# Optimization experiments

Measured on AMD Instinct MI355X. Metric: run time of the kernel, lower is better.

The kernel has to match this reference:

```python
import jax, jax.numpy as jnp
import numpy as np

ENC_H = 128
DEC_H = 256
DEC_STEPS = 10


def _gru_cell(x, h, Wih, Whh, bih, bhh):
    # PyTorch GRU cell, gate order (r, z, n)
    gi = x @ Wih.T + bih          # (B, 3H)
    gh = h @ Whh.T + bhh          # (B, 3H)
    H = h.shape[-1]
    ir, iz, inn = gi[:, :H], gi[:, H:2 * H], gi[:, 2 * H:]
    hr, hz, hn = gh[:, :H], gh[:, H:2 * H], gh[:, 2 * H:]
    r = jax.nn.sigmoid(ir + hr)
    z = jax.nn.sigmoid(iz + hz)
    n = jnp.tanh(inn + r * hn)
    return (1.0 - z) * n + z * h


def setup_inputs() -> dict:
    key = jax.random.key(0)
    ks = jax.random.split(key, 12)
    B, S = 4096, 128
    s = 0.1
    return {
        "x": jax.random.normal(ks[0], (B, S, 5), jnp.float32),
        "y": jax.random.normal(ks[1], (B, S, 1), jnp.float32),
        "enc_Wih": jax.random.normal(ks[2], (3 * ENC_H, 5), jnp.float32) * s,
        "enc_Whh": jax.random.normal(ks[3], (3 * ENC_H, ENC_H), jnp.float32) * s,
        "enc_bih": jax.random.normal(ks[4], (3 * ENC_H,), jnp.float32) * s,
        "enc_bhh": jax.random.normal(ks[5], (3 * ENC_H,), jnp.float32) * s,
        "dec_Wih": jax.random.normal(ks[6], (3 * DEC_H, ENC_H + 1), jnp.float32) * s,
        "dec_Whh": jax.random.normal(ks[7], (3 * DEC_H, DEC_H), jnp.float32) * s,
        "dec_bih": jax.random.normal(ks[8], (3 * DEC_H,), jnp.float32) * s,
        "dec_bhh": jax.random.normal(ks[9], (3 * DEC_H,), jnp.float32) * s,
        "lin_W": jax.random.normal(ks[10], (4, DEC_H), jnp.float32) * s,
        "lin_b": jax.random.normal(ks[11], (4,), jnp.float32) * s,
    }


def reference(x, y, enc_Wih, enc_Whh, enc_bih, enc_bhh,
              dec_Wih, dec_Whh, dec_bih, dec_bhh, lin_W, lin_b):
    B, S, _ = x.shape
    xs = jnp.transpose(x, (1, 0, 2))   # (S, B, 5)
    ys = jnp.transpose(y, (1, 0, 2))   # (S, B, 1)

    # Encoder: only the final hidden state (contex) is consumed downstream.
    h0 = jnp.zeros((B, ENC_H), x.dtype)

    def enc_step(h, xt):
        return _gru_cell(xt, h, enc_Wih, enc_Whh, enc_bih, enc_bhh), None

    contex, _ = jax.lax.scan(enc_step, h0, xs)   # (B, 128)

    # Decoder: initial hidden is ones (torch.ones_like(shape)), 10 steps.
    hdec0 = jnp.ones((B, DEC_H), x.dtype)

    def dec_step(h, yt):
        xt = jnp.concatenate([contex, yt], axis=-1)   # (B, 129)
        h2 = _gru_cell(xt, h, dec_Wih, dec_Whh, dec_bih, dec_bhh)
        out = h2 @ lin_W.T + lin_b                    # (B, 4)
        return h2, out

    _, outs = jax.lax.scan(dec_step, hdec0, ys[:DEC_STEPS])  # (10, B, 4)

    # res starts as ones; only first 10 rows written.
    res = jnp.ones((S, B, 4), x.dtype).at[:DEC_STEPS].set(outs)
    return jnp.transpose(res, (1, 0, 2))   # (B, S, 4)
```

## Files before the change

kernel.cpp:

```cpp
#include <hip/hip_runtime.h>

#define B_SZ 4096
#define S_SZ 128
#define XD 5
#define EH 128
#define DH 256
#define DSTEPS 10

typedef short v8s __attribute__((ext_vector_type(8)));
typedef float v4f __attribute__((ext_vector_type(4)));

__device__ __forceinline__ float bf2f(unsigned short u) {
    union { unsigned int i; float f; } v; v.i = ((unsigned int)u) << 16; return v.f;
}
__device__ __forceinline__ unsigned short f2bf(float f) {
    union { float f; unsigned int i; } v; v.f = f;
    unsigned int x = v.i;
    return (unsigned short)((x + 0x7FFFu + ((x >> 16) & 1u)) >> 16);
}
__device__ __forceinline__ float fexp2(float x) { return __builtin_amdgcn_exp2f(x); }
__device__ __forceinline__ float frcp(float x) { return __builtin_amdgcn_rcpf(x); }
__device__ __forceinline__ unsigned int cvt2bf(float lo, float hi) {
    unsigned int r;
    asm("v_cvt_pk_bf16_f32 %0, %1, %2" : "=v"(r) : "v"(lo), "v"(hi));
    return r;
}

#define SC_S (-1.44269504088896f)
#define SC_T ( 2.88539008177793f)

__global__ __launch_bounds__(256) void prep_kernel(
    const float* __restrict__ dWih,
    const float* __restrict__ dWhh,
    unsigned short* __restrict__ wihp,
    unsigned short* __restrict__ dWhh_bf)
{
    const int gsz = gridDim.x * 256;
    for (int i = blockIdx.x * 256 + threadIdx.x; i < 768 * 256; i += gsz) {
        const float sc = ((i >> 8) < 512) ? SC_S : SC_T;
        dWhh_bf[i] = f2bf(sc * dWhh[i]);
    }
    for (int i = blockIdx.x * 256 + threadIdx.x; i < 768 * 136; i += gsz) {
        int col = i / 136, k = i - col * 136;
        const float sc = (col < 512) ? SC_S : SC_T;
        wihp[i] = (k < 129) ? f2bf(sc * dWih[col * 129 + k]) : (unsigned short)0;
    }
}

__global__ __launch_bounds__(512, 2)
void fused_kernel(
    const float* __restrict__ x,
    const float* __restrict__ Wih32,
    const float* __restrict__ Whh32,
    const float* __restrict__ bih,
    const float* __restrict__ bhh,
    const float* __restrict__ dbih,
    const float* __restrict__ dbhh,
    const float* __restrict__ y,
    const unsigned short* __restrict__ wihp,
    const unsigned short* __restrict__ dWhh_bf,
    const float* __restrict__ linW,
    const float* __restrict__ linb,
    float* __restrict__ out)
{
    __shared__ __align__(16) char uni[118784];
    __shared__ unsigned short hb[2][16][136];
    __shared__ __align__(16) unsigned short zpad[8];
    __shared__ unsigned short hshf[32 * 16 * 8];
    __shared__ unsigned short lwf[32 * 16 * 8];
    __shared__ float ysh[16][DSTEPS];

    const int tid = threadIdx.x;
    const int bid = blockIdx.x;
    const int wv = tid >> 6;
    const int lane = tid & 63;
    const int n = lane & 15;
    const int kg = lane >> 4;
    const int r0 = bid * 16;

    {
        auto xs = (unsigned short (*)[16][8])uni;

        for (int i = tid; i < 2 * 16 * 136; i += 512) ((unsigned short*)hb)[i] = 0;
        if (tid < 8) zpad[tid] = 0;
        for (int i = tid; i < 16 * S_SZ * 8; i += 512) {
            int m = i >> 10;
            int rem = i & 1023;
            int t = rem >> 3;
            int j = rem & 7;
            unsigned short v = 0;
            if (j < XD) v = f2bf(x[(size_t)(r0 + m) * (S_SZ * XD) + t * XD + j]);
            else if (j == XD) v = 0x3F80;
            xs[t][m][j] = v;
        }

        const int colw = wv * 16 + n;
        v8s fw[3][4];
        v8s fx[3];
        #pragma unroll
        for (int g = 0; g < 3; ++g) {
            const float sc = (g < 2) ? SC_S : SC_T;
            const int gcol = g * EH + colw;
            #pragma unroll
            for (int kt = 0; kt < 4; ++kt) {
                const float* p = &Whh32[(size_t)gcol * EH + kt * 32 + kg * 8];
                float4 lo = *(const float4*)p;
                float4 hi = *(const float4*)(p + 4);
                v8s f;
                f[0] = (short)f2bf(sc * lo.x); f[1] = (short)f2bf(sc * lo.y);
                f[2] = (short)f2bf(sc * lo.z); f[3] = (short)f2bf(sc * lo.w);
                f[4] = (short)f2bf(sc * hi.x); f[5] = (short)f2bf(sc * hi.y);
                f[6] = (short)f2bf(sc * hi.z); f[7] = (short)f2bf(sc * hi.w);
                fw[g][kt] = f;
            }
            v8s t = {0, 0, 0, 0, 0, 0, 0, 0};
            if (kg == 0) {
                const float* p = &Wih32[gcol * XD];
                #pragma unroll
                for (int j = 0; j < XD; ++j) t[j] = (short)f2bf(sc * p[j]);
                float b = (g < 2) ? (sc * (bih[gcol] + bhh[gcol]))
                                  : (sc * bih[gcol]);
                t[XD] = (short)f2bf(b);
            }
            fx[g] = t;
        }
        const float bhn = SC_T * bhh[2 * EH + colw];

        const v4f vzero = {0.f, 0.f, 0.f, 0.f};
        float hst[4] = {0.f, 0.f, 0.f, 0.f};
        __syncthreads();

        #pragma unroll 2
        for (int t = 0; t < S_SZ; ++t) {
            const int p = t & 1;
            v8s a[4];
            #pragma unroll
            for (int kt = 0; kt < 4; ++kt)
                a[kt] = *(const v8s*)&hb[p][n][kt * 32 + kg * 8];
            const unsigned short* xsrc = (kg == 0) ? &xs[t][n][0] : &zpad[0];
            v8s ax = *(const v8s*)xsrc;

            v4f accr  = __builtin_amdgcn_mfma_f32_16x16x32_bf16(a[0], fw[0][0], vzero, 0, 0, 0);
            v4f accz  = __builtin_amdgcn_mfma_f32_16x16x32_bf16(a[0], fw[1][0], vzero, 0, 0, 0);
            v4f acchn = __builtin_amdgcn_mfma_f32_16x16x32_bf16(a[0], fw[2][0], vzero, 0, 0, 0);
            #pragma unroll
            for (int kt = 1; kt < 4; ++kt) {
                accr  = __builtin_amdgcn_mfma_f32_16x16x32_bf16(a[kt], fw[0][kt], accr, 0, 0, 0);
                accz  = __builtin_amdgcn_mfma_f32_16x16x32_bf16(a[kt], fw[1][kt], accz, 0, 0, 0);
                acchn = __builtin_amdgcn_mfma_f32_16x16x32_bf16(a[kt], fw[2][kt], acchn, 0, 0, 0);
            }
            accr = __builtin_amdgcn_mfma_f32_16x16x32_bf16(ax, fx[0], accr, 0, 0, 0);
            accz = __builtin_amdgcn_mfma_f32_16x16x32_bf16(ax, fx[1], accz, 0, 0, 0);
            v4f accin = __builtin_amdgcn_mfma_f32_16x16x32_bf16(ax, fx[2], vzero, 0, 0, 0);

            float hnew[4];
            #pragma unroll
            for (int e = 0; e < 4; ++e) {
                float r  = frcp(1.f + fexp2(accr[e]));
                float z  = frcp(1.f + fexp2(accz[e]));
                float nn = 1.f - 2.f * frcp(fexp2(accin[e] + r * (acchn[e] + bhn)) + 1.f);
                float h  = nn + z * (hst[e] - nn);
                hst[e] = h;
                hnew[e] = h;
            }
            const unsigned int pk01 = cvt2bf(hnew[0], hnew[1]);
            const unsigned int pk23 = cvt2bf(hnew[2], hnew[3]);
            hb[1 - p][kg * 4 + 0][colw] = (unsigned short)(pk01 & 0xFFFFu);
            hb[1 - p][kg * 4 + 1][colw] = (unsigned short)(pk01 >> 16);
            hb[1 - p][kg * 4 + 2][colw] = (unsigned short)(pk23 & 0xFFFFu);
            hb[1 - p][kg * 4 + 3][colw] = (unsigned short)(pk23 >> 16);
            __syncthreads();
        }
    }

    {
        const int w = wv;
        const int cbase = w * 32;
        const int rb = r0;
        float* gish = (float*)uni;
        float* wysh = (float*)(uni + 59392);

        {
            int col = tid >> 5, kgrp = tid & 31;
            unsigned short v8[8];
            #pragma unroll
            for (int j = 0; j < 8; ++j)
                v8[j] = (col < 4) ? f2bf(linW[col * 256 + kgrp * 8 + j]) : (unsigned short)0;
            *(uint4*)&lwf[(kgrp * 16 + col) * 8] = *(uint4*)v8;
        }
        if (tid < 16 * DSTEPS) {
            int row = tid / DSTEPS, tt = tid - row * DSTEPS;
            ysh[row][tt] = y[(size_t)(rb + row) * S_SZ + tt];
        }
        for (int i = tid; i < 32 * 16 * 8; i += 512) hshf[i] = 0x3F80;

        v8s fB[3][2][8];
        #pragma unroll
        for (int g = 0; g < 3; ++g)
            #pragma unroll
            for (int cg = 0; cg < 2; ++cg)
                #pragma unroll
                for (int kt = 0; kt < 8; ++kt)
                    fB[g][cg][kt] = *(const v8s*)
                        &dWhh_bf[(size_t)(g * DH + cbase + cg * 16 + n) * DH + kt * 32 + kg * 8];

        const v4f vzero = {0.f, 0.f, 0.f, 0.f};
        v4f gi[3][2];
        #pragma unroll
        for (int g = 0; g < 3; ++g)
            #pragma unroll
            for (int cg = 0; cg < 2; ++cg) gi[g][cg] = vzero;

        #pragma unroll
        for (int kt = 0; kt < 4; ++kt) {
            v8s actex = *(const v8s*)&hb[0][n][kt * 32 + kg * 8];
            #pragma unroll
            for (int g = 0; g < 3; ++g)
                #pragma unroll
                for (int cg = 0; cg < 2; ++cg) {
                    v8s bw = *(const v8s*)
                        &wihp[(size_t)(g * DH + cbase + cg * 16 + n) * 136 + kt * 32 + kg * 8];
                    gi[g][cg] = __builtin_amdgcn_mfma_f32_16x16x32_bf16(bw, actex, gi[g][cg], 0, 0, 0);
                }
        }

        #pragma unroll
        for (int g = 0; g < 3; ++g) {
            const float sc = (g < 2) ? SC_S : SC_T;
            #pragma unroll
            for (int cg = 0; cg < 2; ++cg) {
                #pragma unroll
                for (int e = 0; e < 4; ++e) {
                    const int col = cbase + cg * 16 + kg * 4 + e;
                    const int gcol = g * DH + col;
                    float bb = sc * (dbih[gcol] + ((g < 2) ? dbhh[gcol] : 0.f));
                    gi[g][cg][e] += bb;
                    wysh[tid * 29 + (g * 2 + cg) * 4 + e] = bf2f(wihp[(size_t)gcol * 136 + 128]);
                }
            }
        }
        #pragma unroll
        for (int g = 0; g < 3; ++g)
            #pragma unroll
            for (int cg = 0; cg < 2; ++cg)
                *(v4f*)&gish[tid * 29 + (g * 2 + cg) * 4] = gi[g][cg];
        #pragma unroll
        for (int e = 0; e < 4; ++e) {
            gish[tid * 29 + 24 + e] = SC_T * dbhh[2 * DH + cbase + 0 * 16 + kg * 4 + e];
            wysh[tid * 29 + 24 + e] = SC_T * dbhh[2 * DH + cbase + 1 * 16 + kg * 4 + e];
        }

        const float4 lb4 = *(const float4*)linb;
        float hprev[2][4];
        #pragma unroll
        for (int cg = 0; cg < 2; ++cg)
            #pragma unroll
            for (int e = 0; e < 4; ++e) hprev[cg][e] = 1.0f;

        __syncthreads();

        for (int t = 0; t < DSTEPS; ++t) {
            const float yv = ysh[n][t];

            v4f ar[2], az[2], an[2];
            #pragma unroll
            for (int cg = 0; cg < 2; ++cg) { ar[cg] = vzero; az[cg] = vzero; an[cg] = vzero; }

            #pragma unroll
            for (int kt = 0; kt < 8; ++kt) {
                v8s a = *(const v8s*)&hshf[((kt * 4 + kg) * 16 + n) * 8];
                #pragma unroll
                for (int cg = 0; cg < 2; ++cg) {
                    ar[cg] = __builtin_amdgcn_mfma_f32_16x16x32_bf16(fB[0][cg][kt], a, ar[cg], 0, 0, 0);
                    az[cg] = __builtin_amdgcn_mfma_f32_16x16x32_bf16(fB[1][cg][kt], a, az[cg], 0, 0, 0);
                    an[cg] = __builtin_amdgcn_mfma_f32_16x16x32_bf16(fB[2][cg][kt], a, an[cg], 0, 0, 0);
                }
            }
            __syncthreads();

            #pragma unroll
            for (int cg = 0; cg < 2; ++cg) {
                v4f giR = *(const v4f*)&gish[tid * 29 + (0 * 2 + cg) * 4];
                v4f giZ = *(const v4f*)&gish[tid * 29 + (1 * 2 + cg) * 4];
                v4f giN = *(const v4f*)&gish[tid * 29 + (2 * 2 + cg) * 4];
                v4f wyR = *(const v4f*)&wysh[tid * 29 + (0 * 2 + cg) * 4];
                v4f wyZ = *(const v4f*)&wysh[tid * 29 + (1 * 2 + cg) * 4];
                v4f wyN = *(const v4f*)&wysh[tid * 29 + (2 * 2 + cg) * 4];
                v4f bN  = (cg == 0) ? *(const v4f*)&gish[tid * 29 + 24]
                                    : *(const v4f*)&wysh[tid * 29 + 24];
                float hh[4];
                #pragma unroll
                for (int e = 0; e < 4; ++e) {
                    float r  = frcp(1.f + fexp2(giR[e] + yv * wyR[e] + ar[cg][e]));
                    float z  = frcp(1.f + fexp2(giZ[e] + yv * wyZ[e] + az[cg][e]));
                    float nn = 1.f - 2.f * frcp(
                        fexp2(giN[e] + yv * wyN[e] + r * (an[cg][e] + bN[e])) + 1.f);
                    float h  = nn + z * (hprev[cg][e] - nn);
                    hprev[cg][e] = h;
                    hh[e] = h;
                }
                const unsigned int p01 = cvt2bf(hh[0], hh[1]);
                const unsigned int p23 = cvt2bf(hh[2], hh[3]);
                const int base = cbase + cg * 16 + kg * 4;
                const int idx = (((base >> 3) * 16) + n) * 8 + (base & 7);
                *(uint2*)&hshf[idx] = (uint2){p01, p23};
            }
            __syncthreads();

            if (w == (t & 7)) {
                v4f o4 = vzero;
                #pragma unroll
                for (int kt = 0; kt < 8; ++kt) {
                    v8s a = *(const v8s*)&hshf[((kt * 4 + kg) * 16 + n) * 8];
                    v8s b = *(const v8s*)&lwf[((kt * 4 + kg) * 16 + n) * 8];
                    o4 = __builtin_amdgcn_mfma_f32_16x16x32_bf16(b, a, o4, 0, 0, 0);
                }
                if (kg == 0) {
                    float4 ov = {o4[0] + lb4.x, o4[1] + lb4.y, o4[2] + lb4.z, o4[3] + lb4.w};
                    *(float4*)&out[(size_t)(rb + n) * (S_SZ * 4) + t * 4] = ov;
                }
            }
        }

        for (int j = tid; j < 16 * 512; j += 512) {
            int row = j >> 9, c = j & 511;
            if (c >= DSTEPS * 4) out[(size_t)(rb + row) * 512 + c] = 1.0f;
        }
    }
}

extern "C" void kernel_launch(void* const* d_in, const int* in_sizes, int n_in,
                              void* d_out, int out_size, void* d_ws, size_t ws_size,
                              hipStream_t stream)
{
    const float* x    = (const float*)d_in[0];
    const float* y    = (const float*)d_in[1];
    const float* eWih = (const float*)d_in[2];
    const float* eWhh = (const float*)d_in[3];
    const float* ebih = (const float*)d_in[4];
    const float* ebhh = (const float*)d_in[5];
    const float* dWih = (const float*)d_in[6];
    const float* dWhh = (const float*)d_in[7];
    const float* dbih = (const float*)d_in[8];
    const float* dbhh = (const float*)d_in[9];
    const float* linW = (const float*)d_in[10];
    const float* linb = (const float*)d_in[11];
    float* out = (float*)d_out;

    char* ws = (char*)d_ws;
    unsigned short* wihp    = (unsigned short*)(ws);
    unsigned short* dWhh_bf = (unsigned short*)(ws + 208896);

    prep_kernel<<<256, 256, 0, stream>>>(dWih, dWhh, wihp, dWhh_bf);
    fused_kernel<<<256, 512, 0, stream>>>(x, eWih, eWhh, ebih, ebhh,
                                          dbih, dbhh, y, wihp, dWhh_bf,
                                          linW, linb, out);
}
```

Measured before the change: 235.6 us.

## Double block size to 1024 threads and split decoder columns across 16 waves

Launches the fused kernel with 1024 threads per block. In the encoder only the first 8 waves compute while the others just join the barriers. In the decoder each of the 16 waves now owns 16 hidden columns instead of 32, which halves the per-wave MFMA chain and the register footprint. The goal is to shorten the latency-bound decoder steps. The cost is idle waves in the encoder and 1024-thread barriers, and occupancy can drop because the old 2-blocks-per-CU launch bound is gone.

```diff
diff --git a/kernel.cpp b/kernel.cpp
--- a/kernel.cpp
+++ b/kernel.cpp
@@ -47,7 +47,7 @@
     }
 }
 
-__global__ __launch_bounds__(512, 2)
+__global__ __launch_bounds__(1024)
 void fused_kernel(
     const float* __restrict__ x,
     const float* __restrict__ Wih32,
@@ -81,9 +81,9 @@
     {
         auto xs = (unsigned short (*)[16][8])uni;
 
-        for (int i = tid; i < 2 * 16 * 136; i += 512) ((unsigned short*)hb)[i] = 0;
+        for (int i = tid; i < 2 * 16 * 136; i += 1024) ((unsigned short*)hb)[i] = 0;
         if (tid < 8) zpad[tid] = 0;
-        for (int i = tid; i < 16 * S_SZ * 8; i += 512) {
+        for (int i = tid; i < 16 * S_SZ * 8; i += 1024) {
             int m = i >> 10;
             int rem = i & 1023;
             int t = rem >> 3;
@@ -97,34 +97,37 @@
         const int colw = wv * 16 + n;
         v8s fw[3][4];
         v8s fx[3];
-        #pragma unroll
-        for (int g = 0; g < 3; ++g) {
-            const float sc = (g < 2) ? SC_S : SC_T;
-            const int gcol = g * EH + colw;
-            #pragma unroll
-            for (int kt = 0; kt < 4; ++kt) {
-                const float* p = &Whh32[(size_t)gcol * EH + kt * 32 + kg * 8];
-                float4 lo = *(const float4*)p;
-                float4 hi = *(const float4*)(p + 4);
-                v8s f;
-                f[0] = (short)f2bf(sc * lo.x); f[1] = (short)f2bf(sc * lo.y);
-                f[2] = (short)f2bf(sc * lo.z); f[3] = (short)f2bf(sc * lo.w);
-                f[4] = (short)f2bf(sc * hi.x); f[5] = (short)f2bf(sc * hi.y);
-                f[6] = (short)f2bf(sc * hi.z); f[7] = (short)f2bf(sc * hi.w);
-                fw[g][kt] = f;
-            }
-            v8s t = {0, 0, 0, 0, 0, 0, 0, 0};
-            if (kg == 0) {
-                const float* p = &Wih32[gcol * XD];
-                #pragma unroll
-                for (int j = 0; j < XD; ++j) t[j] = (short)f2bf(sc * p[j]);
-                float b = (g < 2) ? (sc * (bih[gcol] + bhh[gcol]))
-                                  : (sc * bih[gcol]);
-                t[XD] = (short)f2bf(b);
-            }
-            fx[g] = t;
-        }
-        const float bhn = SC_T * bhh[2 * EH + colw];
+        float bhn = 0.f;
+        if (wv < 8) {
+            #pragma unroll
+            for (int g = 0; g < 3; ++g) {
+                const float sc = (g < 2) ? SC_S : SC_T;
+                const int gcol = g * EH + colw;
+                #pragma unroll
+                for (int kt = 0; kt < 4; ++kt) {
+                    const float* p = &Whh32[(size_t)gcol * EH + kt * 32 + kg * 8];
+                    float4 lo = *(const float4*)p;
+                    float4 hi = *(const float4*)(p + 4);
+                    v8s f;
+                    f[0] = (short)f2bf(sc * lo.x); f[1] = (short)f2bf(sc * lo.y);
+                    f[2] = (short)f2bf(sc * lo.z); f[3] = (short)f2bf(sc * lo.w);
+                    f[4] = (short)f2bf(sc * hi.x); f[5] = (short)f2bf(sc * hi.y);
+                    f[6] = (short)f2bf(sc * hi.z); f[7] = (short)f2bf(sc * hi.w);
+                    fw[g][kt] = f;
+                }
+                v8s t = {0, 0, 0, 0, 0, 0, 0, 0};
+                if (kg == 0) {
+                    const float* p = &Wih32[gcol * XD];
+                    #pragma unroll
+                    for (int j = 0; j < XD; ++j) t[j] = (short)f2bf(sc * p[j]);
+                    float b = (g < 2) ? (sc * (bih[gcol] + bhh[gcol]))
+                                      : (sc * bih[gcol]);
+                    t[XD] = (short)f2bf(b);
+                }
+                fx[g] = t;
+            }
+            bhn = SC_T * bhh[2 * EH + colw];
+        }
 
         const v4f vzero = {0.f, 0.f, 0.f, 0.f};
         float hst[4] = {0.f, 0.f, 0.f, 0.f};
@@ -133,54 +136,55 @@
         #pragma unroll 2
         for (int t = 0; t < S_SZ; ++t) {
             const int p = t & 1;
-            v8s a[4];
-            #pragma unroll
-            for (int kt = 0; kt < 4; ++kt)
-                a[kt] = *(const v8s*)&hb[p][n][kt * 32 + kg * 8];
-            const unsigned short* xsrc = (kg == 0) ? &xs[t][n][0] : &zpad[0];
-            v8s ax = *(const v8s*)xsrc;
-
-            v4f accr  = __builtin_amdgcn_mfma_f32_16x16x32_bf16(a[0], fw[0][0], vzero, 0, 0, 0);
-            v4f accz  = __builtin_amdgcn_mfma_f32_16x16x32_bf16(a[0], fw[1][0], vzero, 0, 0, 0);
-            v4f acchn = __builtin_amdgcn_mfma_f32_16x16x32_bf16(a[0], fw[2][0], vzero, 0, 0, 0);
-            #pragma unroll
-            for (int kt = 1; kt < 4; ++kt) {
-                accr  = __builtin_amdgcn_mfma_f32_16x16x32_bf16(a[kt], fw[0][kt], accr, 0, 0, 0);
-                accz  = __builtin_amdgcn_mfma_f32_16x16x32_bf16(a[kt], fw[1][kt], accz, 0, 0, 0);
-                acchn = __builtin_amdgcn_mfma_f32_16x16x32_bf16(a[kt], fw[2][kt], acchn, 0, 0, 0);
-            }
-            accr = __builtin_amdgcn_mfma_f32_16x16x32_bf16(ax, fx[0], accr, 0, 0, 0);
-            accz = __builtin_amdgcn_mfma_f32_16x16x32_bf16(ax, fx[1], accz, 0, 0, 0);
-            v4f accin = __builtin_amdgcn_mfma_f32_16x16x32_bf16(ax, fx[2], vzero, 0, 0, 0);
-
-            float hnew[4];
-            #pragma unroll
-            for (int e = 0; e < 4; ++e) {
-                float r  = frcp(1.f + fexp2(accr[e]));
-                float z  = frcp(1.f + fexp2(accz[e]));
-                float nn = 1.f - 2.f * frcp(fexp2(accin[e] + r * (acchn[e] + bhn)) + 1.f);
-                float h  = nn + z * (hst[e] - nn);
-                hst[e] = h;
-                hnew[e] = h;
-            }
-            const unsigned int pk01 = cvt2bf(hnew[0], hnew[1]);
-            const unsigned int pk23 = cvt2bf(hnew[2], hnew[3]);
-            hb[1 - p][kg * 4 + 0][colw] = (unsigned short)(pk01 & 0xFFFFu);
-            hb[1 - p][kg * 4 + 1][colw] = (unsigned short)(pk01 >> 16);
-            hb[1 - p][kg * 4 + 2][colw] = (unsigned short)(pk23 & 0xFFFFu);
-            hb[1 - p][kg * 4 + 3][colw] = (unsigned short)(pk23 >> 16);
+            if (wv < 8) {
+                v8s a[4];
+                #pragma unroll
+                for (int kt = 0; kt < 4; ++kt)
+                    a[kt] = *(const v8s*)&hb[p][n][kt * 32 + kg * 8];
+                const unsigned short* xsrc = (kg == 0) ? &xs[t][n][0] : &zpad[0];
+                v8s ax = *(const v8s*)xsrc;
+
+                v4f accr  = __builtin_amdgcn_mfma_f32_16x16x32_bf16(a[0], fw[0][0], vzero, 0, 0, 0);
+                v4f accz  = __builtin_amdgcn_mfma_f32_16x16x32_bf16(a[0], fw[1][0], vzero, 0, 0, 0);
+                v4f acchn = __builtin_amdgcn_mfma_f32_16x16x32_bf16(a[0], fw[2][0], vzero, 0, 0, 0);
+                #pragma unroll
+                for (int kt = 1; kt < 4; ++kt) {
+                    accr  = __builtin_amdgcn_mfma_f32_16x16x32_bf16(a[kt], fw[0][kt], accr, 0, 0, 0);
+                    accz  = __builtin_amdgcn_mfma_f32_16x16x32_bf16(a[kt], fw[1][kt], accz, 0, 0, 0);
+                    acchn = __builtin_amdgcn_mfma_f32_16x16x32_bf16(a[kt], fw[2][kt], acchn, 0, 0, 0);
+                }
+                accr = __builtin_amdgcn_mfma_f32_16x16x32_bf16(ax, fx[0], accr, 0, 0, 0);
+                accz = __builtin_amdgcn_mfma_f32_16x16x32_bf16(ax, fx[1], accz, 0, 0, 0);
+                v4f accin = __builtin_amdgcn_mfma_f32_16x16x32_bf16(ax, fx[2], vzero, 0, 0, 0);
+
+                float hnew[4];
+                #pragma unroll
+                for (int e = 0; e < 4; ++e) {
+                    float r  = frcp(1.f + fexp2(accr[e]));
+                    float z  = frcp(1.f + fexp2(accz[e]));
+                    float nn = 1.f - 2.f * frcp(fexp2(accin[e] + r * (acchn[e] + bhn)) + 1.f);
+                    float h  = nn + z * (hst[e] - nn);
+                    hst[e] = h;
+                    hnew[e] = h;
+                }
+                const unsigned int pk01 = cvt2bf(hnew[0], hnew[1]);
+                const unsigned int pk23 = cvt2bf(hnew[2], hnew[3]);
+                hb[1 - p][kg * 4 + 0][colw] = (unsigned short)(pk01 & 0xFFFFu);
+                hb[1 - p][kg * 4 + 1][colw] = (unsigned short)(pk01 >> 16);
+                hb[1 - p][kg * 4 + 2][colw] = (unsigned short)(pk23 & 0xFFFFu);
+                hb[1 - p][kg * 4 + 3][colw] = (unsigned short)(pk23 >> 16);
+            }
             __syncthreads();
         }
     }
 
     {
         const int w = wv;
-        const int cbase = w * 32;
+        const int colb = w * 16;
         const int rb = r0;
-        float* gish = (float*)uni;
-        float* wysh = (float*)(uni + 59392);
-
-        {
+        float* gwsh = (float*)uni;
+
+        if (tid < 512) {
             int col = tid >> 5, kgrp = tid & 31;
             unsigned short v8[8];
             #pragma unroll
@@ -192,122 +196,89 @@
             int row = tid / DSTEPS, tt = tid - row * DSTEPS;
             ysh[row][tt] = y[(size_t)(rb + row) * S_SZ + tt];
         }
-        for (int i = tid; i < 32 * 16 * 8; i += 512) hshf[i] = 0x3F80;
-
-        v8s fB[3][2][8];
+        for (int i = tid; i < 32 * 16 * 8; i += 1024) hshf[i] = 0x3F80;
+
+        v8s fB[3][8];
         #pragma unroll
         for (int g = 0; g < 3; ++g)
             #pragma unroll
-            for (int cg = 0; cg < 2; ++cg)
-                #pragma unroll
-                for (int kt = 0; kt < 8; ++kt)
-                    fB[g][cg][kt] = *(const v8s*)
-                        &dWhh_bf[(size_t)(g * DH + cbase + cg * 16 + n) * DH + kt * 32 + kg * 8];
+            for (int kt = 0; kt < 8; ++kt)
+                fB[g][kt] = *(const v8s*)
+                    &dWhh_bf[(size_t)(g * DH + colb + n) * DH + kt * 32 + kg * 8];
 
         const v4f vzero = {0.f, 0.f, 0.f, 0.f};
-        v4f gi[3][2];
-        #pragma unroll
-        for (int g = 0; g < 3; ++g)
-            #pragma unroll
-            for (int cg = 0; cg < 2; ++cg) gi[g][cg] = vzero;
+        v4f gi[3];
+        #pragma unroll
+        for (int g = 0; g < 3; ++g) gi[g] = vzero;
 
         #pragma unroll
         for (int kt = 0; kt < 4; ++kt) {
             v8s actex = *(const v8s*)&hb[0][n][kt * 32 + kg * 8];
             #pragma unroll
-            for (int g = 0; g < 3; ++g)
-                #pragma unroll
-                for (int cg = 0; cg < 2; ++cg) {
-                    v8s bw = *(const v8s*)
-                        &wihp[(size_t)(g * DH + cbase + cg * 16 + n) * 136 + kt * 32 + kg * 8];
-                    gi[g][cg] = __builtin_amdgcn_mfma_f32_16x16x32_bf16(bw, actex, gi[g][cg], 0, 0, 0);
-                }
+            for (int g = 0; g < 3; ++g) {
+                v8s bw = *(const v8s*)
+                    &wihp[(size_t)(g * DH + colb + n) * 136 + kt * 32 + kg * 8];
+                gi[g] = __builtin_amdgcn_mfma_f32_16x16x32_bf16(bw, actex, gi[g], 0, 0, 0);
+            }
         }
 
         #pragma unroll
         for (int g = 0; g < 3; ++g) {
             const float sc = (g < 2) ? SC_S : SC_T;
             #pragma unroll
-            for (int cg = 0; cg < 2; ++cg) {
-                #pragma unroll
-                for (int e = 0; e < 4; ++e) {
-                    const int col = cbase + cg * 16 + kg * 4 + e;
-                    const int gcol = g * DH + col;
-                    float bb = sc * (dbih[gcol] + ((g < 2) ? dbhh[gcol] : 0.f));
-                    gi[g][cg][e] += bb;
-                    wysh[tid * 29 + (g * 2 + cg) * 4 + e] = bf2f(wihp[(size_t)gcol * 136 + 128]);
-                }
-            }
-        }
-        #pragma unroll
-        for (int g = 0; g < 3; ++g)
-            #pragma unroll
-            for (int cg = 0; cg < 2; ++cg)
-                *(v4f*)&gish[tid * 29 + (g * 2 + cg) * 4] = gi[g][cg];
-        #pragma unroll
-        for (int e = 0; e < 4; ++e) {
-            gish[tid * 29 + 24 + e] = SC_T * dbhh[2 * DH + cbase + 0 * 16 + kg * 4 + e];
-            wysh[tid * 29 + 24 + e] = SC_T * dbhh[2 * DH + cbase + 1 * 16 + kg * 4 + e];
-        }
-
-        const float4 lb4 = *(const float4*)linb;
-        float hprev[2][4];
-        #pragma unroll
-        for (int cg = 0; cg < 2; ++cg)
-            #pragma unroll
-            for (int e = 0; e < 4; ++e) hprev[cg][e] = 1.0f;
-
+            for (int e = 0; e < 4; ++e) {
+                const int gcol = g * DH + colb + kg * 4 + e;
+                gi[g][e] += sc * (dbih[gcol] + ((g < 2) ? dbhh[gcol] : 0.f));
+                gwsh[tid * 29 + 12 + g * 4 + e] = bf2f(wihp[(size_t)gcol * 136 + 128]);
+            }
+            *(v4f*)&gwsh[tid * 29 + g * 4] = gi[g];
+        }
+        #pragma unroll
+        for (int e = 0; e < 4; ++e)
+            gwsh[tid * 29 + 24 + e] = SC_T * dbhh[2 * DH + colb + kg * 4 + e];
+
+        float hprev[4] = {1.f, 1.f, 1.f, 1.f};
         __syncthreads();
 
         for (int t = 0; t < DSTEPS; ++t) {
             const float yv = ysh[n][t];
 
-            v4f ar[2], az[2], an[2];
-            #pragma unroll
-            for (int cg = 0; cg < 2; ++cg) { ar[cg] = vzero; az[cg] = vzero; an[cg] = vzero; }
-
+            v4f ar = vzero, az = vzero, an = vzero;
             #pragma unroll
             for (int kt = 0; kt < 8; ++kt) {
                 v8s a = *(const v8s*)&hshf[((kt * 4 + kg) * 16 + n) * 8];
-                #pragma unroll
-                for (int cg = 0; cg < 2; ++cg) {
-                    ar[cg] = __builtin_amdgcn_mfma_f32_16x16x32_bf16(fB[0][cg][kt], a, ar[cg], 0, 0, 0);
-                    az[cg] = __builtin_amdgcn_mfma_f32_16x16x32_bf16(fB[1][cg][kt], a, az[cg], 0, 0, 0);
-                    an[cg] = __builtin_amdgcn_mfma_f32_16x16x32_bf16(fB[2][cg][kt], a, an[cg], 0, 0, 0);
-                }
+                ar = __builtin_amdgcn_mfma_f32_16x16x32_bf16(fB[0][kt], a, ar, 0, 0, 0);
+                az = __builtin_amdgcn_mfma_f32_16x16x32_bf16(fB[1][kt], a, az, 0, 0, 0);
+                an = __builtin_amdgcn_mfma_f32_16x16x32_bf16(fB[2][kt], a, an, 0, 0, 0);
             }
             __syncthreads();
 
-            #pragma unroll
-            for (int cg = 0; cg < 2; ++cg) {
-                v4f giR = *(const v4f*)&gish[tid * 29 + (0 * 2 + cg) * 4];
-                v4f giZ = *(const v4f*)&gish[tid * 29 + (1 * 2 + cg) * 4];
-                v4f giN = *(const v4f*)&gish[tid * 29 + (2 * 2 + cg) * 4];
-                v4f wyR = *(const v4f*)&wysh[tid * 29 + (0 * 2 + cg) * 4];
-                v4f wyZ = *(const v4f*)&wysh[tid * 29 + (1 * 2 + cg) * 4];
-                v4f wyN = *(const v4f*)&wysh[tid * 29 + (2 * 2 + cg) * 4];
-                v4f bN  = (cg == 0) ? *(const v4f*)&gish[tid * 29 + 24]
-                                    : *(const v4f*)&wysh[tid * 29 + 24];
-                float hh[4];
-                #pragma unroll
-                for (int e = 0; e < 4; ++e) {
-                    float r  = frcp(1.f + fexp2(giR[e] + yv * wyR[e] + ar[cg][e]));
-                    float z  = frcp(1.f + fexp2(giZ[e] + yv * wyZ[e] + az[cg][e]));
-                    float nn = 1.f - 2.f * frcp(
-                        fexp2(giN[e] + yv * wyN[e] + r * (an[cg][e] + bN[e])) + 1.f);
-                    float h  = nn + z * (hprev[cg][e] - nn);
-                    hprev[cg][e] = h;
-                    hh[e] = h;
-                }
-                const unsigned int p01 = cvt2bf(hh[0], hh[1]);
-                const unsigned int p23 = cvt2bf(hh[2], hh[3]);
-                const int base = cbase + cg * 16 + kg * 4;
-                const int idx = (((base >> 3) * 16) + n) * 8 + (base & 7);
-                *(uint2*)&hshf[idx] = (uint2){p01, p23};
-            }
+            float hh[4];
+            #pragma unroll
+            for (int e = 0; e < 4; ++e) {
+                const float giR = gwsh[tid * 29 + 0 + e];
+                const float giZ = gwsh[tid * 29 + 4 + e];
+                const float giN = gwsh[tid * 29 + 8 + e];
+                const float wyR = gwsh[tid * 29 + 12 + e];
+                const float wyZ = gwsh[tid * 29 + 16 + e];
+                const float wyN = gwsh[tid * 29 + 20 + e];
+                const float bN  = gwsh[tid * 29 + 24 + e];
+                float r  = frcp(1.f + fexp2(giR + yv * wyR + ar[e]));
+                float z  = frcp(1.f + fexp2(giZ + yv * wyZ + az[e]));
+                float nn = 1.f - 2.f * frcp(
+                    fexp2(giN + yv * wyN + r * (an[e] + bN)) + 1.f);
+                float h  = nn + z * (hprev[e] - nn);
+                hprev[e] = h;
+                hh[e] = h;
+            }
+            const unsigned int p01 = cvt2bf(hh[0], hh[1]);
+            const unsigned int p23 = cvt2bf(hh[2], hh[3]);
+            const int base = colb + kg * 4;
+            const int idx = (((base >> 3) * 16) + n) * 8 + (base & 7);
+            *(uint2*)&hshf[idx] = (uint2){p01, p23};
             __syncthreads();
 
-            if (w == (t & 7)) {
+            if (w == t) {
                 v4f o4 = vzero;
                 #pragma unroll
                 for (int kt = 0; kt < 8; ++kt) {
@@ -316,13 +287,14 @@
                     o4 = __builtin_amdgcn_mfma_f32_16x16x32_bf16(b, a, o4, 0, 0, 0);
                 }
                 if (kg == 0) {
+                    const float4 lb4 = *(const float4*)linb;
                     float4 ov = {o4[0] + lb4.x, o4[1] + lb4.y, o4[2] + lb4.z, o4[3] + lb4.w};
                     *(float4*)&out[(size_t)(rb + n) * (S_SZ * 4) + t * 4] = ov;
                 }
             }
         }
 
-        for (int j = tid; j < 16 * 512; j += 512) {
+        for (int j = tid; j < 16 * 512; j += 1024) {
             int row = j >> 9, c = j & 511;
             if (c >= DSTEPS * 4) out[(size_t)(rb + row) * 512 + c] = 1.0f;
         }
@@ -352,7 +324,7 @@
     unsigned short* dWhh_bf = (unsigned short*)(ws + 208896);
 
     prep_kernel<<<256, 256, 0, stream>>>(dWih, dWhh, wihp, dWhh_bf);
-    fused_kernel<<<256, 512, 0, stream>>>(x, eWih, eWhh, ebih, ebhh,
-                                          dbih, dbhh, y, wihp, dWhh_bf,
-                                          linW, linb, out);
-}
+    fused_kernel<<<256, 1024, 0, stream>>>(x, eWih, eWhh, ebih, ebhh,
+                                           dbih, dbhh, y, wihp, dWhh_bf,
+                                           linW, linb, out);
+}
```

After: 208.1 us. 1.13x faster.
